# Performance work log

Measured on AMD Instinct MI355X. Metric: run time of the kernel, lower is better.

The kernel has to match this reference:

```python
import jax, jax.numpy as jnp
from jax import lax
import numpy as np

B = 16384
IMG = 28
N = 5                     # code reshaped to 5x5 per sample
K = 2                     # n_principal_components
DN = ('NCHW', 'OIHW', 'NCHW')


def setup_inputs() -> dict:
    key = jax.random.key(0)
    ks = jax.random.split(key, 12)
    p = lambda k, shape, s=0.05: (jax.random.normal(k, shape, jnp.float32) * s)
    return {
        'images': jax.random.normal(ks[0], (B, 1, IMG, IMG), jnp.float32),
        'conv1_w': p(ks[1], (10, 1, 5, 5)),
        'conv1_b': p(ks[2], (10,)),
        'conv2_w': p(ks[3], (20, 10, 5, 5)),
        'conv2_b': p(ks[4], (20,)),
        'lin1_w': p(ks[5], (50, 320)),
        'lin1_b': p(ks[6], (50,)),
        'lin2_w': p(ks[7], (25, 50)),
        'lin2_b': p(ks[8], (25,)),
        'dec1_w': p(ks[9], (160, 25)),
        'dec1_b': p(ks[10], (160,)),
        'dec2_w': p(ks[11], (784, 160)),
        'dec2_b': jnp.zeros((784,), jnp.float32),
    }


def _maxpool2(x):
    return lax.reduce_window(x, -jnp.inf, lax.max, (1, 1, 2, 2), (1, 1, 2, 2), 'VALID')


def reference(images, conv1_w, conv1_b, conv2_w, conv2_b,
              lin1_w, lin1_b, lin2_w, lin2_b,
              dec1_w, dec1_b, dec2_w, dec2_b):
    # ---- encoder ----
    x = lax.conv_general_dilated(images, conv1_w, (1, 1), 'VALID', dimension_numbers=DN)
    x = x + conv1_b[None, :, None, None]          # [B,10,24,24]
    x = jax.nn.selu(_maxpool2(x))                 # [B,10,12,12]
    x = lax.conv_general_dilated(x, conv2_w, (1, 1), 'VALID', dimension_numbers=DN)
    x = x + conv2_b[None, :, None, None]          # [B,20,8,8]
    x = jax.nn.selu(_maxpool2(x))                 # [B,20,4,4]
    x = x.reshape(x.shape[0], -1)                 # [B,320]
    x = jax.nn.selu(x @ lin1_w.T + lin1_b)        # [B,50]
    code = x @ lin2_w.T + lin2_b                  # [B,25]

    # ---- batched 5x5 SVD -> rank-K orthogonal projector ----
    M = code.reshape(-1, N, N)                    # [B,5,5]
    U, _, _ = jnp.linalg.svd(M, full_matrices=False)
    Uk = U[:, :, :K]                              # [B,5,2]
    P = jnp.einsum('bik,bjk->bij', Uk, Uk)        # U_k U_k^T, [B,5,5]
    proj = P.reshape(-1, N * N)                   # [B,25]

    # ---- decoder ----
    h = jax.nn.selu(proj @ dec1_w.T + dec1_b)     # [B,160]
    out = jax.nn.sigmoid(h @ dec2_w.T + dec2_b)   # [B,784]
    out = out.reshape(-1, 1, IMG, IMG)
    return out, code
```

## Files before the change

### kernel.cpp

```cpp
#include <hip/hip_runtime.h>
#include <hip/hip_bf16.h>
#include <math.h>

#define NB 16384

typedef __bf16 bf16x8 __attribute__((ext_vector_type(8)));
typedef __fp16 f16x8  __attribute__((ext_vector_type(8)));
typedef float  f32x4  __attribute__((ext_vector_type(4)));
typedef unsigned short ushort4v __attribute__((ext_vector_type(4)));
typedef unsigned int   uint4v  __attribute__((ext_vector_type(4)));

__device__ __forceinline__ float selu_f(float x) {
    const float kScale = 1.0507009873554805f;
    const float kAlphaScale = 1.7580993408473766f;
    return x > 0.0f ? kScale * x : kAlphaScale * (__expf(x) - 1.0f);
}

__device__ __forceinline__ unsigned short f2bf(float x) {
    unsigned int u = __float_as_uint(x);
    unsigned int r = (u + 0x7FFFu + ((u >> 16) & 1u)) >> 16;
    return (unsigned short)r;
}

__device__ __forceinline__ unsigned int packsplit(float v) {
    const __fp16 h = (__fp16)v;
    const __fp16 l = (__fp16)(v - (float)h);
    const unsigned int hb = (unsigned int)__builtin_bit_cast(unsigned short, h);
    const unsigned int lb = (unsigned int)__builtin_bit_cast(unsigned short, l);
    return hb | (lb << 16);
}

#define PERM_AH 0x05040100u
#define PERM_AL 0x07060302u

union F16x8Cast { uint4v u; f16x8 f; };

#define CH1 145
#define X1SZ (CH1 * 10)
#define IMS 37
#define IMSZ 1064

__device__ __forceinline__ int c2_elem(int s, int g, int j) {
    const int o = s * 4 + g, jp = j >> 1, hl = j & 1;
    if (jp < 3) {
        const int p = o * 3 + jp;
        int ch, idx;
        if (p < 60) { ch = p / 10; idx = p - ch * 10; }
        else        { ch = 6 + (p - 60) / 9; idx = (p - 60) % 9; }
        int tap;
        if (ch < 6)        tap = 5 * (idx >> 1) + 2 * (idx & 1);
        else if (idx == 0) tap = 0;
        else { const int r = ((idx - 1) >> 1) + 1; tap = 5 * r + 2 * ((idx - 1) & 1); }
        return ch * 25 + tap + hl;
    } else {
        const int q = o;
        if (q >= 29) return -1;
        int chp, tap;
        if (q < 15) { chp = q / 5; const int ts = q - chp * 5; tap = 5 * ts + 4; }
        else { const int q2 = q - 15; chp = 3 + q2 / 7; const int ts = q2 % 7;
               tap = (ts < 2) ? (2 + ts) : (5 * (ts - 2) + 4); }
        return (2 * chp + hl) * 25 + tap;
    }
}
__device__ __forceinline__ int c1_elem(int g, int j) {
    const int p = g * 4 + (j >> 1), hl = j & 1;
    if (p < 10) return 5 * (p >> 1) + 2 * (p & 1) + hl;
    if (p < 15) return hl ? -1 : (5 * (p - 10) + 4);
    return -1;
}

__global__ __launch_bounds__(256) void k_prep(
    const float* __restrict__ dec2_w,  unsigned short* __restrict__ wbf,
    const float* __restrict__ lin1_w,  float* __restrict__ lin1_wp,
    const float* __restrict__ conv2_w, unsigned short* __restrict__ woff4,
    __fp16* __restrict__ whi, __fp16* __restrict__ wlo,
    const float* __restrict__ conv1_w, unsigned short* __restrict__ koff4,
    __fp16* __restrict__ whi1, __fp16* __restrict__ wlo1)
{
    int i = blockIdx.x * 256 + threadIdx.x;
    if (i < 125440) { wbf[i] = f2bf(dec2_w[i]); return; }
    i -= 125440;
    if (i < 16000) {
        const int row = i / 320, cn = i - row * 320;
        const int q = cn / 20, oc = cn - q * 20;
        lin1_wp[row * 320 + cn] = lin1_w[row * 320 + oc * 16 + q];
        return;
    }
    i -= 16000;
    if (i < 128) {
        const int s = i >> 4, g = (i >> 2) & 3, jp = i & 3;
        const int e = c2_elem(s, g, jp * 2);
        unsigned short off = 0;
        if (e >= 0) {
            const int ic = e / 25, tap = e - ic * 25;
            off = (unsigned short)(ic * CH1 + (tap / 5) * 12 + tap % 5);
        }
        woff4[i] = off;
        return;
    }
    i -= 128;
    if (i < 16384) {
        const int v = i >> 13;
        const int r = i & 8191;
        const int j = r & 7, lane = (r >> 3) & 63, s = (r >> 9) & 7, nt = r >> 12;
        const int oc = nt * 16 + (lane & 15);
        const int e = c2_elem(s, lane >> 4, j);
        float w = 0.f;
        if (e >= 0 && oc < 20) {
            const int ic = e / 25, tap = e - ic * 25;
            w = conv2_w[(oc * 10 + ic) * 25 + tap];
        }
        const __fp16 hi = (__fp16)w;
        if (v == 0) whi[r] = hi;
        else        wlo[r] = (__fp16)(w - (float)hi);
        return;
    }
    i -= 16384;
    if (i < 16) {
        const int e = c1_elem(i >> 2, (i & 3) * 2);
        koff4[i] = (unsigned short)(e < 0 ? 0 : (e / 5) * IMS + e % 5);
        return;
    }
    i -= 16;
    if (i < 1024) {
        const int v = i >> 9;
        const int r = i & 511;
        const int j = r & 7, lane = r >> 3;
        const int c = lane & 15, g = lane >> 4;
        const int e = c1_elem(g, j);
        const float w = (e >= 0 && c < 10) ? conv1_w[c * 25 + e] : 0.f;
        const __fp16 hi = (__fp16)w;
        if (v == 0) whi1[r] = hi;
        else        wlo1[r] = (__fp16)(w - (float)hi);
    }
}

__global__ __launch_bounds__(256, 4) void k_conv_fused(
    const float* __restrict__ images,
    const float* __restrict__ conv1_b, const float* __restrict__ conv2_b,
    const unsigned short* __restrict__ woff4,
    const __fp16* __restrict__ whi,  const __fp16* __restrict__ wlo,
    const unsigned short* __restrict__ koff4,
    const __fp16* __restrict__ whi1, const __fp16* __restrict__ wlo1,
    float* __restrict__ x2)
{
    __shared__ unsigned int sImgP[4 * IMSZ];
    __shared__ unsigned int sX1P[4 * X1SZ];

    const int t  = threadIdx.x;
    const int b0 = blockIdx.x * 4;

    for (int k = t; k < 4 * 196; k += 256) {
        const int img = k / 196;
        const int r4  = k - img * 196;
        const int row = r4 / 7;
        const int col = (r4 - row * 7) * 4;
        const float4 v = reinterpret_cast<const float4*>(
                             images + (size_t)(b0 + img) * 784)[r4];
        unsigned int* d = sImgP + img * IMSZ + row * IMS + col;
        d[0] = packsplit(v.x); d[1] = packsplit(v.y);
        d[2] = packsplit(v.z); d[3] = packsplit(v.w);
    }
    for (int i = t; i < 112; i += 256) {
        const int img = i / 28, row = i - img * 28;
        sImgP[img * IMSZ + row * IMS + 28] = 0u;
    }
    __syncthreads();

    const int lane = t & 63;
    const int wv   = t >> 6;
    const int g    = lane >> 4;
    const int c0   = lane & 15;

    {
        const unsigned int* imgP = sImgP + wv * IMSZ;
        unsigned int* x1P = sX1P + wv * X1SZ;

        const int sub = c0 & 3, qq = c0 >> 2;
        const int base_lane = (sub >> 1) * IMS + 2 * qq + (sub & 1);
        const ushort4v k4 = *reinterpret_cast<const ushort4v*>(koff4 + g * 4);
        int ab[4];
        #pragma unroll
        for (int jp = 0; jp < 4; ++jp) ab[jp] = base_lane + (int)k4[jp];

        const f16x8 bh1 = *reinterpret_cast<const f16x8*>(whi1 + lane * 8);
        const f16x8 bl1 = *reinterpret_cast<const f16x8*>(wlo1 + lane * 8);
        const float bias = (c0 < 10) ? conv1_b[c0] : 0.f;

        #pragma unroll 1
        for (int a = 0; a < 12; ++a) {
            const int abase = a * (2 * IMS);
            #pragma unroll
            for (int b = 0; b < 3; ++b) {
                const unsigned int* pb_ = imgP + abase + b * 8;
                unsigned int w[8];
                const unsigned int* r0 = pb_ + ab[0]; w[0] = r0[0]; w[1] = r0[1];
                const unsigned int* r1 = pb_ + ab[1]; w[2] = r1[0]; w[3] = r1[1];
                const unsigned int* r2 = pb_ + ab[2]; w[4] = r2[0]; w[5] = r2[1];
                const unsigned int* r3 = pb_ + ab[3]; w[6] = r3[0]; w[7] = r3[1];
                F16x8Cast AH, AL;
                AH.u = (uint4v){ __builtin_amdgcn_perm(w[1], w[0], PERM_AH),
                                 __builtin_amdgcn_perm(w[3], w[2], PERM_AH),
                                 __builtin_amdgcn_perm(w[5], w[4], PERM_AH),
                                 __builtin_amdgcn_perm(w[7], w[6], PERM_AH) };
                AL.u = (uint4v){ __builtin_amdgcn_perm(w[1], w[0], PERM_AL),
                                 __builtin_amdgcn_perm(w[3], w[2], PERM_AL),
                                 __builtin_amdgcn_perm(w[5], w[4], PERM_AL),
                                 __builtin_amdgcn_perm(w[7], w[6], PERM_AL) };
                f32x4 acc = {0.f, 0.f, 0.f, 0.f};
                __builtin_amdgcn_s_setprio(1);
                acc = __builtin_amdgcn_mfma_f32_16x16x32_f16(AH.f, bh1, acc, 0, 0, 0);
                acc = __builtin_amdgcn_mfma_f32_16x16x32_f16(AL.f, bh1, acc, 0, 0, 0);
                acc = __builtin_amdgcn_mfma_f32_16x16x32_f16(AH.f, bl1, acc, 0, 0, 0);
                __builtin_amdgcn_s_setprio(0);
                const float m = fmaxf(fmaxf(acc[0], acc[1]), fmaxf(acc[2], acc[3]));
                if (c0 < 10)
                    x1P[c0 * CH1 + 12 * a + 4 * b + g] = packsplit(selu_f(m + bias));
            }
        }
    }
    __syncthreads();

    {
        const unsigned int* x1P = sX1P + wv * X1SZ;

        int rowbase[4];
        #pragma unroll
        for (int mi = 0; mi < 4; ++mi) {
            const int r64 = mi * 16 + c0;
            const int qi  = r64 >> 2;
            const int sb  = r64 & 3;
            rowbase[mi] = (2 * (qi >> 2) + (sb >> 1)) * 12
                        + 2 * (qi & 3) + (sb & 1);
        }

        f32x4 acc[4][2];
        #pragma unroll
        for (int mi = 0; mi < 4; ++mi) {
            acc[mi][0] = (f32x4){0.f, 0.f, 0.f, 0.f};
            acc[mi][1] = (f32x4){0.f, 0.f, 0.f, 0.f};
        }

        ushort4v of = *reinterpret_cast<const ushort4v*>(woff4 + g * 4);
        f16x8 bh0 = *reinterpret_cast<const f16x8*>(whi + (size_t)(0 * 64 + lane) * 8);
        f16x8 bl0 = *reinterpret_cast<const f16x8*>(wlo + (size_t)(0 * 64 + lane) * 8);
        f16x8 bh1 = *reinterpret_cast<const f16x8*>(whi + (size_t)(8 * 64 + lane) * 8);
        f16x8 bl1 = *reinterpret_cast<const f16x8*>(wlo + (size_t)(8 * 64 + lane) * 8);

        #pragma unroll 1
        for (int s = 0; s < 8; ++s) {
            const int sn = (s + 1) & 7;
            const ushort4v ofn = *reinterpret_cast<const ushort4v*>(woff4 + sn * 16 + g * 4);
            const f16x8 nbh0 = *reinterpret_cast<const f16x8*>(whi + (size_t)((0 + sn) * 64 + lane) * 8);
            const f16x8 nbl0 = *reinterpret_cast<const f16x8*>(wlo + (size_t)((0 + sn) * 64 + lane) * 8);
            const f16x8 nbh1 = *reinterpret_cast<const f16x8*>(whi + (size_t)((8 + sn) * 64 + lane) * 8);
            const f16x8 nbl1 = *reinterpret_cast<const f16x8*>(wlo + (size_t)((8 + sn) * 64 + lane) * 8);

            #pragma unroll
            for (int mi = 0; mi < 4; ++mi) {
                const unsigned int* pp = x1P + rowbase[mi];
                unsigned int w[8];
                const unsigned int* q0 = pp + (int)of[0]; w[0] = q0[0]; w[1] = q0[1];
                const unsigned int* q1 = pp + (int)of[1]; w[2] = q1[0]; w[3] = q1[1];
                const unsigned int* q2 = pp + (int)of[2]; w[4] = q2[0]; w[5] = q2[1];
                const unsigned int* q3 = pp + (int)of[3]; w[6] = q3[0]; w[7] = q3[145];
                F16x8Cast AH, AL;
                AH.u = (uint4v){ __builtin_amdgcn_perm(w[1], w[0], PERM_AH),
                                 __builtin_amdgcn_perm(w[3], w[2], PERM_AH),
                                 __builtin_amdgcn_perm(w[5], w[4], PERM_AH),
                                 __builtin_amdgcn_perm(w[7], w[6], PERM_AH) };
                AL.u = (uint4v){ __builtin_amdgcn_perm(w[1], w[0], PERM_AL),
                                 __builtin_amdgcn_perm(w[3], w[2], PERM_AL),
                                 __builtin_amdgcn_perm(w[5], w[4], PERM_AL),
                                 __builtin_amdgcn_perm(w[7], w[6], PERM_AL) };
                __builtin_amdgcn_s_setprio(1);
                acc[mi][0] = __builtin_amdgcn_mfma_f32_16x16x32_f16(AH.f, bh0, acc[mi][0], 0, 0, 0);
                acc[mi][0] = __builtin_amdgcn_mfma_f32_16x16x32_f16(AL.f, bh0, acc[mi][0], 0, 0, 0);
                acc[mi][0] = __builtin_amdgcn_mfma_f32_16x16x32_f16(AH.f, bl0, acc[mi][0], 0, 0, 0);
                acc[mi][1] = __builtin_amdgcn_mfma_f32_16x16x32_f16(AH.f, bh1, acc[mi][1], 0, 0, 0);
                acc[mi][1] = __builtin_amdgcn_mfma_f32_16x16x32_f16(AL.f, bh1, acc[mi][1], 0, 0, 0);
                acc[mi][1] = __builtin_amdgcn_mfma_f32_16x16x32_f16(AH.f, bl1, acc[mi][1], 0, 0, 0);
                __builtin_amdgcn_s_setprio(0);
            }
            of = ofn; bh0 = nbh0; bl0 = nbl0; bh1 = nbh1; bl1 = nbl1;
        }

        const float bias0 = conv2_b[c0];
        const float bias1 = (c0 < 4) ? conv2_b[16 + c0] : 0.f;
        #pragma unroll
        for (int mi = 0; mi < 4; ++mi) {
            const int qq = mi * 4 + g;
            float* orow = x2 + (size_t)(b0 + wv) * 320 + qq * 20;
            const float v0 = fmaxf(fmaxf(acc[mi][0][0], acc[mi][0][1]),
                                   fmaxf(acc[mi][0][2], acc[mi][0][3]));
            orow[c0] = selu_f(v0 + bias0);
            if (c0 < 4) {
                const float v1 = fmaxf(fmaxf(acc[mi][1][0], acc[mi][1][1]),
                                       fmaxf(acc[mi][1][2], acc[mi][1][3]));
                orow[16 + c0] = selu_f(v1 + bias1);
            }
        }
    }
}

#define NS 16
#define HS 168

__global__ __launch_bounds__(256) void k_tail(
    const float* __restrict__ x2,
    const float* __restrict__ lin1_wp, const float* __restrict__ lin1_b,
    const float* __restrict__ lin2_w,  const float* __restrict__ lin2_b,
    const float* __restrict__ dec1_w,  const float* __restrict__ dec1_b,
    const unsigned short* __restrict__ dec2_wb, const float* __restrict__ dec2_b,
    float* __restrict__ code, float* __restrict__ out)
{
    __shared__ float sIn[NS][324];
    __shared__ float sH[NS][51];
    __shared__ float sC[NS][28];
    __shared__ float sP[NS][26];
    unsigned short* sHd = reinterpret_cast<unsigned short*>(&sIn[0][0]);

    const int t  = threadIdx.x;
    const int b0 = blockIdx.x * NS;

    {
        const float* g = x2 + (size_t)b0 * 320;
        for (int k = t; k < NS * 80; k += 256) {
            const int r  = k / 80;
            const int c4 = k - r * 80;
            reinterpret_cast<float4*>(&sIn[r][0])[c4] =
                reinterpret_cast<const float4*>(g + r * 320)[c4];
        }
    }
    __syncthreads();

    for (int idx = t; idx < NS * 50; idx += 256) {
        const int bi = idx & (NS - 1);
        const int j  = idx / NS;
        float s = lin1_b[j];
        const float4* w  = reinterpret_cast<const float4*>(lin1_wp + j * 320);
        const float4* xi = reinterpret_cast<const float4*>(&sIn[bi][0]);
        #pragma unroll 4
        for (int k4 = 0; k4 < 80; ++k4) {
            const float4 a = xi[k4];
            const float4 wq = w[k4];
            s = fmaf(a.x, wq.x, s); s = fmaf(a.y, wq.y, s);
            s = fmaf(a.z, wq.z, s); s = fmaf(a.w, wq.w, s);
        }
        sH[bi][j] = selu_f(s);
    }
    __syncthreads();
    for (int idx = t; idx < NS * 25; idx += 256) {
        const int bi = idx & (NS - 1);
        const int j  = idx / NS;
        float s = lin2_b[j];
        const float* w = lin2_w + j * 50;
        #pragma unroll
        for (int k = 0; k < 50; ++k) s = fmaf(sH[bi][k], w[k], s);
        code[(size_t)(b0 + bi) * 25 + j] = s;
        sC[bi][j] = s;
    }
    __syncthreads();

    if (t < NS) {
        float M[5][5];
        #pragma unroll
        for (int i = 0; i < 5; ++i)
            #pragma unroll
            for (int j = 0; j < 5; ++j) M[i][j] = sC[t][i * 5 + j];

        float A[5][5], V[5][5];
        #pragma unroll
        for (int i = 0; i < 5; ++i) {
            #pragma unroll
            for (int j = 0; j < 5; ++j) {
                float s = 0.f;
                #pragma unroll
                for (int k = 0; k < 5; ++k) s = fmaf(M[i][k], M[j][k], s);
                A[i][j] = s;
                V[i][j] = (i == j) ? 1.f : 0.f;
            }
        }
        for (int sweep = 0; sweep < 6; ++sweep) {
            #pragma unroll
            for (int p = 0; p < 4; ++p) {
                #pragma unroll
                for (int q = p + 1; q < 5; ++q) {
                    const float apq = A[p][q];
                    if (fabsf(apq) > 1e-30f) {
                        const float app = A[p][p], aqq = A[q][q];
                        const float tau = (aqq - app) / (2.f * apq);
                        const float tt  = (tau >= 0.f ? 1.f : -1.f) /
                                          (fabsf(tau) + sqrtf(1.f + tau * tau));
                        const float cc  = 1.f / sqrtf(1.f + tt * tt);
                        const float ss  = tt * cc;
                        #pragma unroll
                        for (int i = 0; i < 5; ++i) {
                            if (i == p || i == q) continue;
                            const float aip = A[i][p], aiq = A[i][q];
                            A[i][p] = A[p][i] = cc * aip - ss * aiq;
                            A[i][q] = A[q][i] = ss * aip + cc * aiq;
                        }
                        A[p][p] = app - tt * apq;
                        A[q][q] = aqq + tt * apq;
                        A[p][q] = A[q][p] = 0.f;
                        #pragma unroll
                        for (int i = 0; i < 5; ++i) {
                            const float vip = V[i][p], viq = V[i][q];
                            V[i][p] = cc * vip - ss * viq;
                            V[i][q] = ss * vip + cc * viq;
                        }
                    }
                }
            }
        }
        float d[5];
        #pragma unroll
        for (int i = 0; i < 5; ++i) d[i] = A[i][i];
        float sel[5];
        #pragma unroll
        for (int c1 = 0; c1 < 5; ++c1) {
            int cnt = 0;
            #pragma unroll
            for (int c2 = 0; c2 < 5; ++c2) {
                if (c2 == c1) continue;
                if (d[c2] > d[c1] || (d[c2] == d[c1] && c2 < c1)) ++cnt;
            }
            sel[c1] = (cnt < 2) ? 1.f : 0.f;
        }
        #pragma unroll
        for (int i = 0; i < 5; ++i) {
            #pragma unroll
            for (int j = 0; j < 5; ++j) {
                float s = 0.f;
                #pragma unroll
                for (int k = 0; k < 5; ++k) s = fmaf(sel[k] * V[i][k], V[j][k], s);
                sP[t][i * 5 + j] = s;
            }
        }
    }
    __syncthreads();

    const int bi = t & (NS - 1);
    const int j0 = t / NS;
    {
        float p[25];
        #pragma unroll
        for (int k = 0; k < 25; ++k) p[k] = sP[bi][k];
        #pragma unroll 2
        for (int i = 0; i < 10; ++i) {
            const int j = j0 + i * 16;
            const float* w = dec1_w + j * 25;
            float s = dec1_b[j];
            #pragma unroll
            for (int k = 0; k < 25; ++k) s = fmaf(p[k], w[k], s);
            sHd[bi * HS + j] = f2bf(selu_f(s));
        }
    }
    __syncthreads();

    const int wv   = t >> 6;
    const int lane = t & 63;
    const int arow = lane & 15;
    const int kgrp = lane >> 4;

    bf16x8 afr[5];
    #pragma unroll
    for (int ks = 0; ks < 5; ++ks)
        afr[ks] = *reinterpret_cast<const bf16x8*>(
            &sHd[arow * HS + ks * 32 + kgrp * 8]);

    for (int ct = wv; ct < 49; ct += 4) {
        const int col = ct * 16 + arow;
        bf16x8 bfr[5];
        const unsigned short* wp = dec2_wb + (size_t)col * 160 + kgrp * 8;
        #pragma unroll
        for (int ks = 0; ks < 5; ++ks)
            bfr[ks] = *reinterpret_cast<const bf16x8*>(wp + ks * 32);

        f32x4 acc0 = {0.f, 0.f, 0.f, 0.f};
        #pragma unroll
        for (int ks = 0; ks < 5; ++ks)
            acc0 = __builtin_amdgcn_mfma_f32_16x16x32_bf16(afr[ks], bfr[ks], acc0, 0, 0, 0);
        const float bb = dec2_b[col];
        #pragma unroll
        for (int r = 0; r < 4; ++r) {
            const int row = kgrp * 4 + r;
            const float v0 = acc0[r] + bb;
            out[(size_t)(b0 + row) * 784 + col] = 1.0f / (1.0f + __expf(-v0));
        }
    }
}

extern "C" void kernel_launch(void* const* d_in, const int* in_sizes, int n_in,
                              void* d_out, int out_size, void* d_ws, size_t ws_size,
                              hipStream_t stream) {
    const float* images  = (const float*)d_in[0];
    const float* conv1_w = (const float*)d_in[1];
    const float* conv1_b = (const float*)d_in[2];
    const float* conv2_w = (const float*)d_in[3];
    const float* conv2_b = (const float*)d_in[4];
    const float* lin1_w  = (const float*)d_in[5];
    const float* lin1_b  = (const float*)d_in[6];
    const float* lin2_w  = (const float*)d_in[7];
    const float* lin2_b  = (const float*)d_in[8];
    const float* dec1_w  = (const float*)d_in[9];
    const float* dec1_b  = (const float*)d_in[10];
    const float* dec2_w  = (const float*)d_in[11];
    const float* dec2_b  = (const float*)d_in[12];

    float* out_img = (float*)d_out;
    float* code    = (float*)d_out + (size_t)NB * 784;

    char* ws = (char*)d_ws;
    float*          x2      = (float*)ws;
    unsigned short* wbf     = (unsigned short*)(ws + (size_t)NB * 345 * 4);
    char*           pB      = ws + (size_t)NB * 345 * 4 + 250880;
    float*          lin1_wp = (float*)pB;
    unsigned short* woff4   = (unsigned short*)(pB + 64000);
    __fp16*         whi     = (__fp16*)(pB + 64512);
    __fp16*         wlo     = (__fp16*)(pB + 80896);
    unsigned short* koff4   = (unsigned short*)(pB + 97280);
    __fp16*         whi1    = (__fp16*)(pB + 97344);
    __fp16*         wlo1    = (__fp16*)(pB + 98368);

    k_prep     <<<622,      256, 0, stream>>>(dec2_w, wbf, lin1_w, lin1_wp,
                                              conv2_w, woff4, whi, wlo,
                                              conv1_w, koff4, whi1, wlo1);
    k_conv_fused<<<NB / 4,  256, 0, stream>>>(images, conv1_b, conv2_b,
                                              woff4, whi, wlo,
                                              koff4, whi1, wlo1, x2);
    k_tail     <<<NB / NS, 256, 0, stream>>>(x2, lin1_wp, lin1_b,
                                             lin2_w, lin2_b,
                                             dec1_w, dec1_b,
                                             wbf, dec2_b,
                                             code, out_img);
}
```

Baseline: 166.7 us.

## Compute lin1 layer with split-fp16 MFMA and pre-split conv2 activations

The 320->50 lin1 layer in the tail kernel moves from scalar FP32 FMAs over shared memory to 16x16x32 f16 MFMAs. Precision is kept with a hi/lo fp16 split: weights are pre-split into interleaved fragments in the prep kernel, and the conv kernel now writes its activations already packed as hi/lo pairs. The scalar loop over 50 outputs by 16 samples and its FP32 weight reads are replaced by a few MFMAs per wave. The Jacobi SVD skip test also changes from an absolute threshold to a relative one, which can skip more rotations but alters numerics slightly.

```diff
diff --git a/kernel.cpp b/kernel.cpp
--- a/kernel.cpp
+++ b/kernel.cpp
@@ -71,7 +71,8 @@
 
 __global__ __launch_bounds__(256) void k_prep(
     const float* __restrict__ dec2_w,  unsigned short* __restrict__ wbf,
-    const float* __restrict__ lin1_w,  float* __restrict__ lin1_wp,
+    const float* __restrict__ lin1_w,  __fp16* __restrict__ whiL,
+    __fp16* __restrict__ wloL,
     const float* __restrict__ conv2_w, unsigned short* __restrict__ woff4,
     __fp16* __restrict__ whi, __fp16* __restrict__ wlo,
     const float* __restrict__ conv1_w, unsigned short* __restrict__ koff4,
@@ -80,13 +81,20 @@
     int i = blockIdx.x * 256 + threadIdx.x;
     if (i < 125440) { wbf[i] = f2bf(dec2_w[i]); return; }
     i -= 125440;
-    if (i < 16000) {
-        const int row = i / 320, cn = i - row * 320;
-        const int q = cn / 20, oc = cn - q * 20;
-        lin1_wp[row * 320 + cn] = lin1_w[row * 320 + oc * 16 + q];
+    if (i < 20480) {
+        const int j = i & 7, lane = (i >> 3) & 63, rest = i >> 9;
+        const int nt = rest / 10, ks = rest - nt * 10;
+        const int k    = ks * 32 + ((lane >> 4) & 3) * 8 + j;
+        const int ocol = nt * 16 + (lane & 15);
+        float w = 0.f;
+        if (ocol < 50)
+            w = lin1_w[ocol * 320 + (k % 20) * 16 + (k / 20)];
+        const __fp16 hi = (__fp16)w;
+        whiL[i] = hi;
+        wloL[i] = (__fp16)(w - (float)hi);
         return;
     }
-    i -= 16000;
+    i -= 20480;
     if (i < 128) {
         const int s = i >> 4, g = (i >> 2) & 3, jp = i & 3;
         const int e = c2_elem(s, g, jp * 2);
@@ -142,7 +150,7 @@
     const __fp16* __restrict__ whi,  const __fp16* __restrict__ wlo,
     const unsigned short* __restrict__ koff4,
     const __fp16* __restrict__ whi1, const __fp16* __restrict__ wlo1,
-    float* __restrict__ x2)
+    unsigned int* __restrict__ x2p)
 {
     __shared__ unsigned int sImgP[4 * IMSZ];
     __shared__ unsigned int sX1P[4 * X1SZ];
@@ -290,14 +298,14 @@
         #pragma unroll
         for (int mi = 0; mi < 4; ++mi) {
             const int qq = mi * 4 + g;
-            float* orow = x2 + (size_t)(b0 + wv) * 320 + qq * 20;
+            unsigned int* orow = x2p + (size_t)(b0 + wv) * 320 + qq * 20;
             const float v0 = fmaxf(fmaxf(acc[mi][0][0], acc[mi][0][1]),
                                    fmaxf(acc[mi][0][2], acc[mi][0][3]));
-            orow[c0] = selu_f(v0 + bias0);
+            orow[c0] = packsplit(selu_f(v0 + bias0));
             if (c0 < 4) {
                 const float v1 = fmaxf(fmaxf(acc[mi][1][0], acc[mi][1][1]),
                                        fmaxf(acc[mi][1][2], acc[mi][1][3]));
-                orow[16 + c0] = selu_f(v1 + bias1);
+                orow[16 + c0] = packsplit(selu_f(v1 + bias1));
             }
         }
     }
@@ -305,51 +313,74 @@
 
 #define NS 16
 #define HS 168
+#define SIS 324
 
 __global__ __launch_bounds__(256) void k_tail(
-    const float* __restrict__ x2,
-    const float* __restrict__ lin1_wp, const float* __restrict__ lin1_b,
+    const unsigned int* __restrict__ x2p,
+    const __fp16* __restrict__ whiL, const __fp16* __restrict__ wloL,
+    const float* __restrict__ lin1_b,
     const float* __restrict__ lin2_w,  const float* __restrict__ lin2_b,
     const float* __restrict__ dec1_w,  const float* __restrict__ dec1_b,
     const unsigned short* __restrict__ dec2_wb, const float* __restrict__ dec2_b,
     float* __restrict__ code, float* __restrict__ out)
 {
-    __shared__ float sIn[NS][324];
+    __shared__ unsigned int sInP[NS][SIS];
     __shared__ float sH[NS][51];
     __shared__ float sC[NS][28];
     __shared__ float sP[NS][26];
-    unsigned short* sHd = reinterpret_cast<unsigned short*>(&sIn[0][0]);
+    unsigned short* sHd = reinterpret_cast<unsigned short*>(&sInP[0][0]);
 
     const int t  = threadIdx.x;
     const int b0 = blockIdx.x * NS;
+    const int lane = t & 63;
+    const int wv   = t >> 6;
 
     {
-        const float* g = x2 + (size_t)b0 * 320;
+        const uint4v* g = reinterpret_cast<const uint4v*>(x2p + (size_t)b0 * 320);
         for (int k = t; k < NS * 80; k += 256) {
             const int r  = k / 80;
             const int c4 = k - r * 80;
-            reinterpret_cast<float4*>(&sIn[r][0])[c4] =
-                reinterpret_cast<const float4*>(g + r * 320)[c4];
-        }
-    }
-    __syncthreads();
-
-    for (int idx = t; idx < NS * 50; idx += 256) {
-        const int bi = idx & (NS - 1);
-        const int j  = idx / NS;
-        float s = lin1_b[j];
-        const float4* w  = reinterpret_cast<const float4*>(lin1_wp + j * 320);
-        const float4* xi = reinterpret_cast<const float4*>(&sIn[bi][0]);
-        #pragma unroll 4
-        for (int k4 = 0; k4 < 80; ++k4) {
-            const float4 a = xi[k4];
-            const float4 wq = w[k4];
-            s = fmaf(a.x, wq.x, s); s = fmaf(a.y, wq.y, s);
-            s = fmaf(a.z, wq.z, s); s = fmaf(a.w, wq.w, s);
-        }
-        sH[bi][j] = selu_f(s);
-    }
-    __syncthreads();
+            *reinterpret_cast<uint4v*>(&sInP[r][c4 * 4]) = g[k];
+        }
+    }
+    __syncthreads();
+
+    const int arow = lane & 15;
+    const int kgrp = lane >> 4;
+    {
+        f32x4 accL = {0.f, 0.f, 0.f, 0.f};
+        #pragma unroll 1
+        for (int ks = 0; ks < 10; ++ks) {
+            const unsigned int* pa = &sInP[arow][ks * 32 + kgrp * 8];
+            const uint4v w0 = *reinterpret_cast<const uint4v*>(pa);
+            const uint4v w1 = *reinterpret_cast<const uint4v*>(pa + 4);
+            F16x8Cast AH, AL;
+            AH.u = (uint4v){ __builtin_amdgcn_perm(w0[1], w0[0], PERM_AH),
+                             __builtin_amdgcn_perm(w0[3], w0[2], PERM_AH),
+                             __builtin_amdgcn_perm(w1[1], w1[0], PERM_AH),
+                             __builtin_amdgcn_perm(w1[3], w1[2], PERM_AH) };
+            AL.u = (uint4v){ __builtin_amdgcn_perm(w0[1], w0[0], PERM_AL),
+                             __builtin_amdgcn_perm(w0[3], w0[2], PERM_AL),
+                             __builtin_amdgcn_perm(w1[1], w1[0], PERM_AL),
+                             __builtin_amdgcn_perm(w1[3], w1[2], PERM_AL) };
+            const f16x8 bh = *reinterpret_cast<const f16x8*>(
+                whiL + ((size_t)(wv * 10 + ks) * 64 + lane) * 8);
+            const f16x8 bl = *reinterpret_cast<const f16x8*>(
+                wloL + ((size_t)(wv * 10 + ks) * 64 + lane) * 8);
+            accL = __builtin_amdgcn_mfma_f32_16x16x32_f16(AH.f, bh, accL, 0, 0, 0);
+            accL = __builtin_amdgcn_mfma_f32_16x16x32_f16(AL.f, bh, accL, 0, 0, 0);
+            accL = __builtin_amdgcn_mfma_f32_16x16x32_f16(AH.f, bl, accL, 0, 0, 0);
+        }
+        const int ocol = wv * 16 + arow;
+        if (ocol < 50) {
+            const float bb = lin1_b[ocol];
+            #pragma unroll
+            for (int r = 0; r < 4; ++r)
+                sH[kgrp * 4 + r][ocol] = selu_f(accL[r] + bb);
+        }
+    }
+    __syncthreads();
+
     for (int idx = t; idx < NS * 25; idx += 256) {
         const int bi = idx & (NS - 1);
         const int j  = idx / NS;
@@ -387,8 +418,8 @@
                 #pragma unroll
                 for (int q = p + 1; q < 5; ++q) {
                     const float apq = A[p][q];
-                    if (fabsf(apq) > 1e-30f) {
-                        const float app = A[p][p], aqq = A[q][q];
+                    const float app = A[p][p], aqq = A[q][q];
+                    if (apq * apq > 1e-13f * fmaxf(app * aqq, 1e-30f)) {
                         const float tau = (aqq - app) / (2.f * apq);
                         const float tt  = (tau >= 0.f ? 1.f : -1.f) /
                                           (fabsf(tau) + sqrtf(1.f + tau * tau));
@@ -459,11 +490,6 @@
     }
     __syncthreads();
 
-    const int wv   = t >> 6;
-    const int lane = t & 63;
-    const int arow = lane & 15;
-    const int kgrp = lane >> 4;
-
     bf16x8 afr[5];
     #pragma unroll
     for (int ks = 0; ks < 5; ++ks)
@@ -513,24 +539,25 @@
     float* code    = (float*)d_out + (size_t)NB * 784;
 
     char* ws = (char*)d_ws;
-    float*          x2      = (float*)ws;
-    unsigned short* wbf     = (unsigned short*)(ws + (size_t)NB * 345 * 4);
-    char*           pB      = ws + (size_t)NB * 345 * 4 + 250880;
-    float*          lin1_wp = (float*)pB;
-    unsigned short* woff4   = (unsigned short*)(pB + 64000);
-    __fp16*         whi     = (__fp16*)(pB + 64512);
-    __fp16*         wlo     = (__fp16*)(pB + 80896);
-    unsigned short* koff4   = (unsigned short*)(pB + 97280);
-    __fp16*         whi1    = (__fp16*)(pB + 97344);
-    __fp16*         wlo1    = (__fp16*)(pB + 98368);
-
-    k_prep     <<<622,      256, 0, stream>>>(dec2_w, wbf, lin1_w, lin1_wp,
+    unsigned int*   x2p     = (unsigned int*)ws;
+    unsigned short* wbf     = (unsigned short*)(ws + (size_t)NB * 320 * 4);
+    char*           pB      = ws + (size_t)NB * 320 * 4 + 250880;
+    __fp16*         whiL    = (__fp16*)pB;
+    __fp16*         wloL    = (__fp16*)(pB + 40960);
+    unsigned short* woff4   = (unsigned short*)(pB + 81920);
+    __fp16*         whi     = (__fp16*)(pB + 82432);
+    __fp16*         wlo     = (__fp16*)(pB + 98816);
+    unsigned short* koff4   = (unsigned short*)(pB + 115200);
+    __fp16*         whi1    = (__fp16*)(pB + 115264);
+    __fp16*         wlo1    = (__fp16*)(pB + 116288);
+
+    k_prep     <<<639,      256, 0, stream>>>(dec2_w, wbf, lin1_w, whiL, wloL,
                                               conv2_w, woff4, whi, wlo,
                                               conv1_w, koff4, whi1, wlo1);
     k_conv_fused<<<NB / 4,  256, 0, stream>>>(images, conv1_b, conv2_b,
                                               woff4, whi, wlo,
-                                              koff4, whi1, wlo1, x2);
-    k_tail     <<<NB / NS, 256, 0, stream>>>(x2, lin1_wp, lin1_b,
+                                              koff4, whi1, wlo1, x2p);
+    k_tail     <<<NB / NS, 256, 0, stream>>>(x2p, whiL, wloL, lin1_b,
                                              lin2_w, lin2_b,
                                              dec1_w, dec1_b,
                                              wbf, dec2_b,
```

Measured after the change: 139.1 us. 16.6% less time.
